# Kernel optimization log

Measured on AMD Instinct MI355X. Metric: run time of the kernel, lower is better.

## Reference

```python
import jax, jax.numpy as jnp
import numpy as np

VOCAB = 32000
HID = 1024
IN_DIM = 768
LAYERS = 2


def setup_inputs() -> dict:
    key = jax.random.key(0)
    ks = jax.random.split(key, 12)
    s = 0.02
    B, N, S = 8, 16, 512
    return {
        "concepts": jax.random.normal(ks[0], (B, N, IN_DIM), dtype=jnp.float32),
        "target_sequence": jax.random.randint(ks[1], (B, S), 0, VOCAB),
        "embedding": s * jax.random.normal(ks[2], (VOCAB, HID), dtype=jnp.float32),
        "w_ih": s * jax.random.normal(ks[3], (LAYERS, 3 * HID, HID), dtype=jnp.float32),
        "w_hh": s * jax.random.normal(ks[4], (LAYERS, 3 * HID, HID), dtype=jnp.float32),
        "b_ih": jnp.zeros((LAYERS, 3 * HID), dtype=jnp.float32),
        "b_hh": jnp.zeros((LAYERS, 3 * HID), dtype=jnp.float32),
        "fc_w": s * jax.random.normal(ks[5], (VOCAB, HID), dtype=jnp.float32),
        "fc_b": jnp.zeros((VOCAB,), dtype=jnp.float32),
        "c2h_w": s * jax.random.normal(ks[6], (HID * LAYERS, IN_DIM), dtype=jnp.float32),
        "c2h_b": jnp.zeros((HID * LAYERS,), dtype=jnp.float32),
    }


def _gru_layer(x, h0, w_ih, w_hh, b_ih, b_hh):
    # x: [B,S,H], h0: [B,H]. PyTorch GRU gate order: r, z, n.
    xg = jnp.einsum('bsh,gh->bsg', x, w_ih) + b_ih  # precompute input gates [B,S,3H]

    def step(h, xg_t):
        hg = h @ w_hh.T + b_hh
        xr, xz, xn = jnp.split(xg_t, 3, axis=-1)
        hr, hz, hn = jnp.split(hg, 3, axis=-1)
        r = jax.nn.sigmoid(xr + hr)
        z = jax.nn.sigmoid(xz + hz)
        n = jnp.tanh(xn + r * hn)
        h_new = (1.0 - z) * n + z * h
        return h_new, h_new

    _, ys = jax.lax.scan(step, h0, jnp.swapaxes(xg, 0, 1))  # [S,B,H]
    return jnp.swapaxes(ys, 0, 1)


def reference(concepts, target_sequence, embedding, w_ih, w_hh, b_ih, b_hh,
              fc_w, fc_b, c2h_w, c2h_b):
    B = concepts.shape[0]
    global_context = jnp.mean(concepts, axis=1)  # [B, D]
    h0 = (global_context @ c2h_w.T + c2h_b).reshape(B, LAYERS, HID)
    h0 = jnp.swapaxes(h0, 0, 1)  # [L, B, H] matching torch view(L, B, H)
    x = embedding[target_sequence]  # [B, S, H]
    for l in range(LAYERS):
        x = _gru_layer(x, h0[l], w_ih[l], w_hh[l], b_ih[l], b_hh[l])
    logits = jnp.einsum('bsh,vh->bsv', x, fc_w) + fc_b
    return logits
```

## Files before the change

kernel.cpp:

```cpp
#include <hip/hip_runtime.h>
#include <hip/hip_bf16.h>
#include <stdint.h>

#define B_ 8
#define S_ 512
#define H_ 1024
#define V_ 32000
#define D_ 768
#define G3H (3*H_)

typedef __bf16 bf16x8_t __attribute__((ext_vector_type(8)));
typedef float f32x4_t __attribute__((ext_vector_type(4)));

__device__ __forceinline__ unsigned short f2bf(float f) {
  unsigned int u = __float_as_uint(f);
  u += 0x7fffu + ((u >> 16) & 1u);
  return (unsigned short)(u >> 16);
}
__device__ __forceinline__ float fast_sigmoid(float x) {
  float e = __builtin_amdgcn_exp2f(x * -1.44269504088896340736f);
  return __builtin_amdgcn_rcpf(1.0f + e);
}
__device__ __forceinline__ float fast_tanh(float x) {
  float e = __builtin_amdgcn_exp2f(x * -2.88539008177792681472f);
  return 2.0f * __builtin_amdgcn_rcpf(1.0f + e) - 1.0f;
}

__global__ void zero_buf(uint4* __restrict__ p, int n) {
  int i = blockIdx.x * 256 + threadIdx.x;
  if (i < n) p[i] = uint4{0, 0, 0, 0};
}

__global__ void ctx_mean(const float* __restrict__ c, float* __restrict__ ctx) {
  int b = blockIdx.x;
  for (int d = threadIdx.x; d < D_; d += 256) {
    float s = 0.f;
    #pragma unroll
    for (int n = 0; n < 16; ++n) s += c[((size_t)b * 16 + n) * D_ + d];
    ctx[b * D_ + d] = s * (1.0f / 16.0f);
  }
}

__global__ void h0_compute(const float* __restrict__ ctx, const float* __restrict__ w,
                           const float* __restrict__ bias, float* __restrict__ h0l,
                           unsigned short* __restrict__ hb) {
  int o = blockIdx.x * 256 + threadIdx.x;
  int b = o >> 11, row = o & 2047;
  float s = bias[row];
  const float* cw = w + (size_t)row * D_;
  const float* cb = ctx + b * D_;
  for (int d = 0; d < D_; ++d) s += cb[d] * cw[d];
  int layer = row >> 10, u = row & 1023;
  h0l[((size_t)layer * 8 + b) * 1024 + u] = s;
  hb[(layer ? 24576 : 0) + b * 1024 + u] = f2bf(s);
}

__global__ void gather_embed(const int* __restrict__ seq, const float* __restrict__ emb,
                             unsigned short* __restrict__ x) {
  int r = blockIdx.x;
  int idx = seq[r];
  float4 v = ((const float4*)(emb + (size_t)idx * H_))[threadIdx.x];
  ushort4 o;
  o.x = f2bf(v.x); o.y = f2bf(v.y); o.z = f2bf(v.z); o.w = f2bf(v.w);
  ((ushort4*)(x + (size_t)r * H_))[threadIdx.x] = o;
}

__global__ void f32_to_bf16(const float* __restrict__ in, unsigned short* __restrict__ outp, long n4) {
  long i = blockIdx.x * (long)blockDim.x + threadIdx.x;
  long stride = (long)gridDim.x * blockDim.x;
  for (; i < n4; i += stride) {
    float4 v = ((const float4*)in)[i];
    ushort4 o;
    o.x = f2bf(v.x); o.y = f2bf(v.y); o.z = f2bf(v.z); o.w = f2bf(v.w);
    ((ushort4*)outp)[i] = o;
  }
}

__global__ __launch_bounds__(256) void gemm_bt_bf16(
    const unsigned short* __restrict__ A, const unsigned short* __restrict__ B,
    float* __restrict__ C, const float* __restrict__ bias,
    int M, int N, int K)
{
  __shared__ __align__(16) unsigned short As[128 * 32];
  __shared__ __align__(16) unsigned short Bs[128 * 32];
  const int tid = threadIdx.x;
  const int l = tid & 63;
  const int w = tid >> 6;
  const int wr = w >> 1, wc = w & 1;
  const long row0 = (long)blockIdx.y * 128;
  const long col0 = (long)blockIdx.x * 128;

  f32x4_t acc[4][4];
  #pragma unroll
  for (int m = 0; m < 4; ++m)
    #pragma unroll
    for (int n = 0; n < 4; ++n) acc[m][n] = (f32x4_t)0.0f;

  const int sr = tid >> 2;
  const int sc = (tid & 3) << 3;

  for (int kt = 0; kt < K; kt += 32) {
    __syncthreads();
    uint4 a0 = *(const uint4*)&A[(row0 + sr) * K + kt + sc];
    uint4 a1 = *(const uint4*)&A[(row0 + sr + 64) * K + kt + sc];
    uint4 b0 = *(const uint4*)&B[(col0 + sr) * K + kt + sc];
    uint4 b1 = *(const uint4*)&B[(col0 + sr + 64) * K + kt + sc];
    ((uint4*)As)[tid]       = a0;
    ((uint4*)As)[tid + 256] = a1;
    ((uint4*)Bs)[tid]       = b0;
    ((uint4*)Bs)[tid + 256] = b1;
    __syncthreads();

    bf16x8_t af[4], bfr[4];
    #pragma unroll
    for (int m = 0; m < 4; ++m)
      af[m] = *(const bf16x8_t*)&As[(wr * 64 + m * 16 + (l & 15)) * 32 + (l >> 4) * 8];
    #pragma unroll
    for (int n = 0; n < 4; ++n)
      bfr[n] = *(const bf16x8_t*)&Bs[(wc * 64 + n * 16 + (l & 15)) * 32 + (l >> 4) * 8];
    #pragma unroll
    for (int m = 0; m < 4; ++m)
      #pragma unroll
      for (int n = 0; n < 4; ++n)
        acc[m][n] = __builtin_amdgcn_mfma_f32_16x16x32_bf16(af[m], bfr[n], acc[m][n], 0, 0, 0);
  }

  #pragma unroll
  for (int n = 0; n < 4; ++n) {
    const long col = col0 + wc * 64 + n * 16 + (l & 15);
    const float bv = bias[col];
    #pragma unroll
    for (int m = 0; m < 4; ++m) {
      const long rbase = row0 + wr * 64 + m * 16 + ((l >> 4) << 2);
      #pragma unroll
      for (int v = 0; v < 4; ++v)
        C[(rbase + v) * (long)N + col] = acc[m][n][v] + bv;
    }
  }
}

__device__ __forceinline__ void load_wfrag3(const float* __restrict__ W, int j0, int w,
                                            int l15, int lhi, bf16x8_t wf[3][8]) {
  #pragma unroll
  for (int m = 0; m < 3; ++m) {
    const float* pr = W + (size_t)((m << 10) + j0 + l15) * 1024 + (w << 8) + (lhi << 3);
    #pragma unroll
    for (int c = 0; c < 8; ++c) {
      f32x4_t v0 = *(const f32x4_t*)(pr + (c << 5));
      f32x4_t v1 = *(const f32x4_t*)(pr + (c << 5) + 4);
      bf16x8_t f;
      f[0] = (__bf16)v0[0]; f[1] = (__bf16)v0[1]; f[2] = (__bf16)v0[2]; f[3] = (__bf16)v0[3];
      f[4] = (__bf16)v1[0]; f[5] = (__bf16)v1[1]; f[6] = (__bf16)v1[2]; f[7] = (__bf16)v1[3];
      wf[m][c] = f;
    }
  }
}

__global__ __launch_bounds__(256, 1) void gru_fused(
    const float* __restrict__ xg,
    const float* __restrict__ w_hh,
    const float* __restrict__ w_ih,
    const float* __restrict__ b_hh,
    const float* __restrict__ b_ih,
    const float* __restrict__ h0f,
    unsigned short* __restrict__ y,
    unsigned short* __restrict__ hb,
    int* __restrict__ fl)
{
  __shared__ __align__(16) float red[4 * 4 * 256];
  const int tid = threadIdx.x;
  const int blk = blockIdx.x;
  const int layer = blk >> 6;
  const int j0 = (blk & 63) << 4;
  const int w = tid >> 6;
  const int l = tid & 63;
  const int l15 = l & 15;
  const int lhi = l >> 4;
  const bool realrow = (l15 < 8);

  bf16x8_t wfh[3][8], wfi[3][8];
  #pragma unroll
  for (int m = 0; m < 3; ++m)
    #pragma unroll
    for (int c = 0; c < 8; ++c) wfi[m][c] = (bf16x8_t)(__bf16)0.0f;
  load_wfrag3(w_hh + (size_t)layer * G3H * H_, j0, w, l15, lhi, wfh);
  if (layer == 1) load_wfrag3(w_ih + (size_t)G3H * H_, j0, w, l15, lhi, wfi);

  const int up = tid & 7;
  const int b = tid >> 3;
  float gbr0 = 0.f, gbz0 = 0.f, gbnh0 = 0.f, gbni0 = 0.f, hp0 = 0.f;
  float gbr1 = 0.f, gbz1 = 0.f, gbnh1 = 0.f, gbni1 = 0.f, hp1 = 0.f;
  const float* xgp = nullptr;
  if (tid < 64) {
    const float* bhh_l = b_hh + (size_t)layer * G3H;
    const float* bih_l = b_ih + (size_t)layer * G3H;
    const int uj = j0 + 2 * up;
    float bhr0 = bhh_l[uj],     bhz0 = bhh_l[1024 + uj],     bhn0 = bhh_l[2048 + uj];
    float bhr1 = bhh_l[uj + 1], bhz1 = bhh_l[1024 + uj + 1], bhn1 = bhh_l[2048 + uj + 1];
    if (layer == 0) {
      gbr0 = bhr0; gbz0 = bhz0; gbnh0 = bhn0;
      gbr1 = bhr1; gbz1 = bhz1; gbnh1 = bhn1;
      xgp = xg + (size_t)(b * S_) * G3H + uj;
    } else {
      gbr0 = bhr0 + bih_l[uj];     gbz0 = bhz0 + bih_l[1024 + uj];
      gbnh0 = bhn0;                gbni0 = bih_l[2048 + uj];
      gbr1 = bhr1 + bih_l[uj + 1]; gbz1 = bhz1 + bih_l[1024 + uj + 1];
      gbnh1 = bhn1;                gbni1 = bih_l[2048 + uj + 1];
    }
    float2 h2 = *(const float2*)&h0f[(size_t)layer * 8192 + b * 1024 + uj];
    hp0 = h2.x; hp1 = h2.y;
  }

  unsigned short* const hb0 = hb;
  unsigned short* const hb1 = hb + 24576;
  const int frag = l15 * 1024 + (w << 8) + (lhi << 3);

  for (int e = 0; e <= S_; ++e) {
    const bool active = (layer == 0) ? (e < S_) : (e >= 1);
    const int t = (layer == 0) ? e : (e - 1);
    const int s3 = e % 3;

    if (tid >= 64 && tid < 192) {
      const int idx = tid - 64;
      const int thr = (idx < 64) ? e : ((layer == 0) ? (e - 1) : e);
      while (__hip_atomic_load(&fl[idx * 32], __ATOMIC_RELAXED, __HIP_MEMORY_SCOPE_AGENT) < thr)
        __builtin_amdgcn_s_sleep(1);
    }
    __syncthreads();

    f32x4_t accR = (f32x4_t)0.0f, accZ = (f32x4_t)0.0f;
    f32x4_t accNh = (f32x4_t)0.0f, accNi = (f32x4_t)0.0f;
    float2 xr2 = {0.f, 0.f}, xz2 = {0.f, 0.f}, xn2 = {0.f, 0.f};

    if (active) {
      f32x4_t hv[8], yv[8];
      #pragma unroll
      for (int c = 0; c < 8; ++c) { hv[c] = (f32x4_t)0.0f; yv[c] = (f32x4_t)0.0f; }
      if (realrow) {
        const unsigned short* hp = (layer == 0) ? (hb0 + s3 * 8192 + frag)
                                                : (hb1 + ((e + 1) & 1) * 8192 + frag);
        #pragma unroll
        for (int c = 0; c < 8; ++c)
          asm volatile("global_load_dwordx4 %0, %1, off offset:%2 sc0 sc1"
                       : "=v"(hv[c]) : "v"(hp), "i"(c * 64) : "memory");
        if (layer == 1) {
          const unsigned short* yp = hb0 + s3 * 8192 + frag;
          #pragma unroll
          for (int c = 0; c < 8; ++c)
            asm volatile("global_load_dwordx4 %0, %1, off offset:%2 sc0 sc1"
                         : "=v"(yv[c]) : "v"(yp), "i"(c * 64) : "memory");
        }
      }
      if (layer == 0 && tid < 64) {
        const float* p = xgp + (size_t)t * G3H;
        xr2 = *(const float2*)p;
        xz2 = *(const float2*)(p + 1024);
        xn2 = *(const float2*)(p + 2048);
      }
      asm volatile("s_waitcnt vmcnt(0)" ::: "memory");
      __builtin_amdgcn_sched_barrier(0);

      #pragma unroll
      for (int c = 0; c < 8; ++c) {
        bf16x8_t hf = __builtin_bit_cast(bf16x8_t, hv[c]);
        accR  = __builtin_amdgcn_mfma_f32_16x16x32_bf16(wfh[0][c], hf, accR,  0, 0, 0);
        accZ  = __builtin_amdgcn_mfma_f32_16x16x32_bf16(wfh[1][c], hf, accZ,  0, 0, 0);
        accNh = __builtin_amdgcn_mfma_f32_16x16x32_bf16(wfh[2][c], hf, accNh, 0, 0, 0);
      }
      if (layer == 1) {
        #pragma unroll
        for (int c = 0; c < 8; ++c) {
          bf16x8_t yf = __builtin_bit_cast(bf16x8_t, yv[c]);
          accR  = __builtin_amdgcn_mfma_f32_16x16x32_bf16(wfi[0][c], yf, accR,  0, 0, 0);
          accZ  = __builtin_amdgcn_mfma_f32_16x16x32_bf16(wfi[1][c], yf, accZ,  0, 0, 0);
          accNi = __builtin_amdgcn_mfma_f32_16x16x32_bf16(wfi[2][c], yf, accNi, 0, 0, 0);
        }
      }
      *(f32x4_t*)&red[(w * 4 + 0) * 256 + (l << 2)] = accR;
      *(f32x4_t*)&red[(w * 4 + 1) * 256 + (l << 2)] = accZ;
      *(f32x4_t*)&red[(w * 4 + 2) * 256 + (l << 2)] = accNh;
      *(f32x4_t*)&red[(w * 4 + 3) * 256 + (l << 2)] = accNi;
    }
    __syncthreads();

    if (active && tid < 64) {
      const int u0 = 2 * up, u1 = 2 * up + 1;
      const int i0 = ((((u0 >> 2) << 4) | b) << 2) + (u0 & 3);
      const int i1 = ((((u1 >> 2) << 4) | b) << 2) + (u1 & 3);
      float aR0 = 0.f, aZ0 = 0.f, aNh0 = 0.f, aNi0 = 0.f;
      float aR1 = 0.f, aZ1 = 0.f, aNh1 = 0.f, aNi1 = 0.f;
      #pragma unroll
      for (int ww = 0; ww < 4; ++ww) {
        const float* rw = red + ww * 1024;
        aR0  += rw[i0];        aR1  += rw[i1];
        aZ0  += rw[256 + i0];  aZ1  += rw[256 + i1];
        aNh0 += rw[512 + i0];  aNh1 += rw[512 + i1];
        aNi0 += rw[768 + i0];  aNi1 += rw[768 + i1];
      }
      float r0, z0, n0, r1, z1, n1;
      if (layer == 0) {
        r0 = fast_sigmoid(xr2.x + gbr0 + aR0);
        z0 = fast_sigmoid(xz2.x + gbz0 + aZ0);
        n0 = fast_tanh(xn2.x + r0 * (aNh0 + gbnh0));
        r1 = fast_sigmoid(xr2.y + gbr1 + aR1);
        z1 = fast_sigmoid(xz2.y + gbz1 + aZ1);
        n1 = fast_tanh(xn2.y + r1 * (aNh1 + gbnh1));
      } else {
        r0 = fast_sigmoid(aR0 + gbr0);
        z0 = fast_sigmoid(aZ0 + gbz0);
        n0 = fast_tanh(aNi0 + gbni0 + r0 * (aNh0 + gbnh0));
        r1 = fast_sigmoid(aR1 + gbr1);
        z1 = fast_sigmoid(aZ1 + gbz1);
        n1 = fast_tanh(aNi1 + gbni1 + r1 * (aNh1 + gbnh1));
      }
      hp0 = (1.0f - z0) * n0 + z0 * hp0;
      hp1 = (1.0f - z1) * n1 + z1 * hp1;
      uint32_t word = ((uint32_t)f2bf(hp1) << 16) | (uint32_t)f2bf(hp0);
      unsigned short* hdst = (layer == 0)
          ? (hb0 + ((e + 1) % 3) * 8192 + b * 1024 + j0 + 2 * up)
          : (hb1 + (e & 1) * 8192 + b * 1024 + j0 + 2 * up);
      if (layer == 1)
        *(uint32_t*)&y[(((size_t)(b * S_ + t)) << 10) + j0 + 2 * up] = word;
      asm volatile("global_store_dword %0, %1, off sc0 sc1"
                   :: "v"(hdst), "v"(word) : "memory");
    }
    asm volatile("s_waitcnt vmcnt(0)" ::: "memory");
    if (tid == 0)
      __hip_atomic_store(&fl[blk * 32], e + 1,
                         __ATOMIC_RELAXED, __HIP_MEMORY_SCOPE_AGENT);
  }
}

extern "C" void kernel_launch(void* const* d_in, const int* in_sizes, int n_in,
                              void* d_out, int out_size, void* d_ws, size_t ws_size,
                              hipStream_t stream) {
  (void)in_sizes; (void)n_in; (void)out_size; (void)ws_size;
  const float* concepts = (const float*)d_in[0];
  const int*   seq      = (const int*)d_in[1];
  const float* emb      = (const float*)d_in[2];
  const float* w_ih     = (const float*)d_in[3];
  const float* w_hh     = (const float*)d_in[4];
  const float* b_ih     = (const float*)d_in[5];
  const float* b_hh     = (const float*)d_in[6];
  const float* fc_w     = (const float*)d_in[7];
  const float* fc_b     = (const float*)d_in[8];
  const float* c2h_w    = (const float*)d_in[9];
  const float* c2h_b    = (const float*)d_in[10];
  float* out = (float*)d_out;

  char* ws = (char*)d_ws;
  size_t off = 0;
  auto alloc = [&](size_t bytes) {
    char* p = ws + off;
    off += (bytes + 255) & ~(size_t)255;
    return p;
  };
  unsigned short* xy   = (unsigned short*)alloc((size_t)B_ * S_ * H_ * 2);
  float*          xg   = (float*)alloc((size_t)B_ * S_ * G3H * 4);
  unsigned short* wihb = (unsigned short*)alloc((size_t)G3H * H_ * 2);
  unsigned short* fcwb = (unsigned short*)alloc((size_t)V_ * H_ * 2);
  float*          ctx  = (float*)alloc((size_t)B_ * D_ * 4);
  float*          h0l  = (float*)alloc((size_t)2 * B_ * H_ * 4);
  unsigned short* hb   = (unsigned short*)alloc((size_t)5 * 8 * 1024 * 2);
  int*            fl   = (int*)alloc((size_t)128 * 32 * 4);

  zero_buf<<<dim3(4), dim3(256), 0, stream>>>((uint4*)fl, 128 * 32 / 4);
  ctx_mean<<<dim3(8), dim3(256), 0, stream>>>(concepts, ctx);
  h0_compute<<<dim3(64), dim3(256), 0, stream>>>(ctx, c2h_w, c2h_b, h0l, hb);
  gather_embed<<<dim3(B_ * S_), dim3(256), 0, stream>>>(seq, emb, xy);
  f32_to_bf16<<<dim3(1024), dim3(256), 0, stream>>>(w_ih, wihb, (long)G3H * H_ / 4);
  f32_to_bf16<<<dim3(2048), dim3(256), 0, stream>>>(fc_w, fcwb, (long)V_ * H_ / 4);

  gemm_bt_bf16<<<dim3(G3H / 128, (B_ * S_) / 128), dim3(256), 0, stream>>>(
      xy, wihb, xg, b_ih, B_ * S_, G3H, H_);

  gru_fused<<<dim3(128), dim3(256), 0, stream>>>(
      xg, w_hh, w_ih, b_hh, b_ih, h0l, xy, hb, fl);

  gemm_bt_bf16<<<dim3(V_ / 128, (B_ * S_) / 128), dim3(256), 0, stream>>>(
      xy, fcwb, out, fc_b, B_ * S_, V_, H_);
}
```

Baseline: 2.505 ms.

## Tag hidden-state words with step ids to replace flag barriers in GRU recurrence

The persistent GRU kernel now splits work across 256 blocks of 8 hidden units each instead of 128 blocks of 16. It packs the gate rows into two MFMA tiles, so less of each tile is padding. Each published hidden-state value carries a 32-bit step tag, so consumers poll the data itself until all tags match. This replaces the per-block flag spin-waits and the store-drain before signalling. A flag is kept only to stop layer 0 from running too far ahead of layer 1, using a 4-deep ring. The trade-off is twice the bytes per hidden-state read, retry loops over the loads, and a correctness risk if the tag scheme or ring depth is wrong.

```diff
diff --git a/kernel.cpp b/kernel.cpp
--- a/kernel.cpp
+++ b/kernel.cpp
@@ -43,16 +43,21 @@
 
 __global__ void h0_compute(const float* __restrict__ ctx, const float* __restrict__ w,
                            const float* __restrict__ bias, float* __restrict__ h0l,
-                           unsigned short* __restrict__ hb) {
+                           uint32_t* __restrict__ hb0, uint32_t* __restrict__ hb1) {
   int o = blockIdx.x * 256 + threadIdx.x;
-  int b = o >> 11, row = o & 2047;
-  float s = bias[row];
-  const float* cw = w + (size_t)row * D_;
+  int layer = o >> 12, b = (o >> 9) & 7, p = o & 511;
+  int row = layer * 1024 + 2 * p;
+  float s0 = bias[row], s1 = bias[row + 1];
   const float* cb = ctx + b * D_;
-  for (int d = 0; d < D_; ++d) s += cb[d] * cw[d];
-  int layer = row >> 10, u = row & 1023;
-  h0l[((size_t)layer * 8 + b) * 1024 + u] = s;
-  hb[(layer ? 24576 : 0) + b * 1024 + u] = f2bf(s);
+  const float* w0 = w + (size_t)row * D_;
+  const float* w1 = w0 + D_;
+  for (int d = 0; d < D_; ++d) { s0 += cb[d] * w0[d]; s1 += cb[d] * w1[d]; }
+  h0l[layer * 8192 + b * 1024 + 2 * p] = s0;
+  h0l[layer * 8192 + b * 1024 + 2 * p + 1] = s1;
+  uint32_t vals = ((uint32_t)f2bf(s1) << 16) | (uint32_t)f2bf(s0);
+  uint32_t* dst = (layer ? hb1 : hb0) + ((size_t)b * 512 + p) * 2;
+  dst[0] = vals;
+  dst[1] = 0u;
 }
 
 __global__ void gather_embed(const int* __restrict__ seq, const float* __restrict__ emb,
@@ -139,21 +144,32 @@
   }
 }
 
-__device__ __forceinline__ void load_wfrag3(const float* __restrict__ W, int j0, int w,
-                                            int l15, int lhi, bf16x8_t wf[3][8]) {
+__device__ __forceinline__ void load_wfrag(const float* __restrict__ W, int j0, int w,
+                                           int l15, int lhi, bf16x8_t wf[2][8]) {
   #pragma unroll
-  for (int m = 0; m < 3; ++m) {
-    const float* pr = W + (size_t)((m << 10) + j0 + l15) * 1024 + (w << 8) + (lhi << 3);
+  for (int m = 0; m < 2; ++m) {
+    const int idx = m * 16 + l15;
+    const int gg = idx >> 3, uu = idx & 7;
     #pragma unroll
     for (int c = 0; c < 8; ++c) {
-      f32x4_t v0 = *(const f32x4_t*)(pr + (c << 5));
-      f32x4_t v1 = *(const f32x4_t*)(pr + (c << 5) + 4);
+      f32x4_t v0 = {0.f, 0.f, 0.f, 0.f}, v1 = {0.f, 0.f, 0.f, 0.f};
+      if (idx < 24) {
+        const float* p = W + (size_t)((gg << 10) + j0 + uu) * 1024
+                           + (w << 8) + (c << 5) + (lhi << 3);
+        v0 = *(const f32x4_t*)p;
+        v1 = *(const f32x4_t*)(p + 4);
+      }
       bf16x8_t f;
       f[0] = (__bf16)v0[0]; f[1] = (__bf16)v0[1]; f[2] = (__bf16)v0[2]; f[3] = (__bf16)v0[3];
       f[4] = (__bf16)v1[0]; f[5] = (__bf16)v1[1]; f[6] = (__bf16)v1[2]; f[7] = (__bf16)v1[3];
       wf[m][c] = f;
     }
   }
+}
+
+__device__ __forceinline__ bf16x8_t pack_frag(const uint4 a, const uint4 b) {
+  uint4 r; r.x = a.x; r.y = a.z; r.z = b.x; r.w = b.z;
+  return __builtin_bit_cast(bf16x8_t, r);
 }
 
 __global__ __launch_bounds__(256, 1) void gru_fused(
@@ -164,34 +180,35 @@
     const float* __restrict__ b_ih,
     const float* __restrict__ h0f,
     unsigned short* __restrict__ y,
-    unsigned short* __restrict__ hb,
+    uint32_t* __restrict__ hb0,
+    uint32_t* __restrict__ hb1,
     int* __restrict__ fl)
 {
-  __shared__ __align__(16) float red[4 * 4 * 256];
+  __shared__ __align__(16) float red[2 * 4 * 3 * 256];
   const int tid = threadIdx.x;
   const int blk = blockIdx.x;
-  const int layer = blk >> 6;
-  const int j0 = (blk & 63) << 4;
+  const int layer = blk >> 7;
+  const int j0 = (blk & 127) * 8;
   const int w = tid >> 6;
   const int l = tid & 63;
   const int l15 = l & 15;
   const int lhi = l >> 4;
   const bool realrow = (l15 < 8);
 
-  bf16x8_t wfh[3][8], wfi[3][8];
+  bf16x8_t wfh[2][8], wfi[2][8];
   #pragma unroll
-  for (int m = 0; m < 3; ++m)
+  for (int m = 0; m < 2; ++m)
     #pragma unroll
     for (int c = 0; c < 8; ++c) wfi[m][c] = (bf16x8_t)(__bf16)0.0f;
-  load_wfrag3(w_hh + (size_t)layer * G3H * H_, j0, w, l15, lhi, wfh);
-  if (layer == 1) load_wfrag3(w_ih + (size_t)G3H * H_, j0, w, l15, lhi, wfi);
-
-  const int up = tid & 7;
-  const int b = tid >> 3;
+  load_wfrag(w_hh + (size_t)layer * G3H * H_, j0, w, l15, lhi, wfh);
+  if (layer == 1) load_wfrag(w_ih + (size_t)G3H * H_, j0, w, l15, lhi, wfi);
+
+  const int up = tid & 3;
+  const int bb = tid >> 2;
   float gbr0 = 0.f, gbz0 = 0.f, gbnh0 = 0.f, gbni0 = 0.f, hp0 = 0.f;
   float gbr1 = 0.f, gbz1 = 0.f, gbnh1 = 0.f, gbni1 = 0.f, hp1 = 0.f;
   const float* xgp = nullptr;
-  if (tid < 64) {
+  if (tid < 32) {
     const float* bhh_l = b_hh + (size_t)layer * G3H;
     const float* bih_l = b_ih + (size_t)layer * G3H;
     const int uj = j0 + 2 * up;
@@ -200,102 +217,179 @@
     if (layer == 0) {
       gbr0 = bhr0; gbz0 = bhz0; gbnh0 = bhn0;
       gbr1 = bhr1; gbz1 = bhz1; gbnh1 = bhn1;
-      xgp = xg + (size_t)(b * S_) * G3H + uj;
+      xgp = xg + (size_t)(bb * S_) * G3H + uj;
     } else {
       gbr0 = bhr0 + bih_l[uj];     gbz0 = bhz0 + bih_l[1024 + uj];
       gbnh0 = bhn0;                gbni0 = bih_l[2048 + uj];
       gbr1 = bhr1 + bih_l[uj + 1]; gbz1 = bhz1 + bih_l[1024 + uj + 1];
       gbnh1 = bhn1;                gbni1 = bih_l[2048 + uj + 1];
     }
-    float2 h2 = *(const float2*)&h0f[(size_t)layer * 8192 + b * 1024 + uj];
+    float2 h2 = *(const float2*)&h0f[(size_t)layer * 8192 + bb * 1024 + uj];
     hp0 = h2.x; hp1 = h2.y;
   }
 
-  unsigned short* const hb0 = hb;
-  unsigned short* const hb1 = hb + 24576;
-  const int frag = l15 * 1024 + (w << 8) + (lhi << 3);
+  const int lane_off = ((l15 << 9) + (w << 7) + (lhi << 2)) * 2;
+  const bool fduty = (layer == 0) && (tid >= 64 && tid < 192);
+  int* flp = fl + (tid - 64) * 32;
+
+  __syncthreads();
 
   for (int e = 0; e <= S_; ++e) {
-    const bool active = (layer == 0) ? (e < S_) : (e >= 1);
+    const bool act = (layer == 0) ? (e < S_) : (e >= 1);
     const int t = (layer == 0) ? e : (e - 1);
-    const int s3 = e % 3;
-
-    if (tid >= 64 && tid < 192) {
-      const int idx = tid - 64;
-      const int thr = (idx < 64) ? e : ((layer == 0) ? (e - 1) : e);
-      while (__hip_atomic_load(&fl[idx * 32], __ATOMIC_RELAXED, __HIP_MEMORY_SCOPE_AGENT) < thr)
-        __builtin_amdgcn_s_sleep(1);
+    const int p = e & 1;
+
+    f32x4_t a0h = (f32x4_t)0.0f, a1h = (f32x4_t)0.0f, a1i = (f32x4_t)0.0f;
+    float2 xr2 = {0.f, 0.f}, xz2 = {0.f, 0.f}, xn2 = {0.f, 0.f};
+    int flv = 0x7fffffff;
+
+    if (act) {
+      if (layer == 0) {
+        if (fduty)
+          asm volatile("global_load_dword %0, %1, off sc0 sc1"
+                       : "=v"(flv) : "v"(flp) : "memory");
+        if (tid < 32) {
+          const float* xp = xgp + (size_t)t * G3H;
+          xr2 = *(const float2*)xp;
+          xz2 = *(const float2*)(xp + 1024);
+          xn2 = *(const float2*)(xp + 2048);
+        }
+        const uint32_t* rb = hb0 + (size_t)(e & 3) * 8192 + lane_off;
+        const uint32_t tg = (uint32_t)e;
+        uint4 q0[8], q1[8];
+        #pragma unroll
+        for (int c = 0; c < 8; ++c) { q0[c] = uint4{0,0,0,0}; q1[c] = uint4{0,0,0,0}; }
+        if (realrow) {
+          #pragma unroll
+          for (int c = 0; c < 8; ++c)
+            asm volatile("global_load_dwordx4 %0, %2, off offset:%3 sc0 sc1\n\t"
+                         "global_load_dwordx4 %1, %2, off offset:%4 sc0 sc1"
+                         : "=&v"(q0[c]), "=&v"(q1[c])
+                         : "v"(rb), "i"(c * 128), "i"(c * 128 + 16) : "memory");
+        }
+        asm volatile("s_waitcnt vmcnt(0)" ::: "memory");
+        __builtin_amdgcn_sched_barrier(0);
+        for (;;) {
+          uint32_t bad = 0;
+          if (realrow) {
+            #pragma unroll
+            for (int c = 0; c < 8; ++c)
+              bad |= (q0[c].y ^ tg) | (q0[c].w ^ tg) | (q1[c].y ^ tg) | (q1[c].w ^ tg);
+          }
+          if (!__any(bad != 0)) break;
+          if (realrow) {
+            #pragma unroll
+            for (int c = 0; c < 8; ++c)
+              asm volatile("global_load_dwordx4 %0, %2, off offset:%3 sc0 sc1\n\t"
+                           "global_load_dwordx4 %1, %2, off offset:%4 sc0 sc1"
+                           : "=&v"(q0[c]), "=&v"(q1[c])
+                           : "v"(rb), "i"(c * 128), "i"(c * 128 + 16) : "memory");
+          }
+          asm volatile("s_waitcnt vmcnt(0)" ::: "memory");
+          __builtin_amdgcn_sched_barrier(0);
+        }
+        if (fduty) {
+          while (flv < e - 3) {
+            __builtin_amdgcn_s_sleep(1);
+            flv = __hip_atomic_load(flp, __ATOMIC_RELAXED, __HIP_MEMORY_SCOPE_AGENT);
+          }
+        }
+        __builtin_amdgcn_sched_barrier(0);
+        #pragma unroll
+        for (int c = 0; c < 8; ++c) {
+          bf16x8_t hf = pack_frag(q0[c], q1[c]);
+          a0h = __builtin_amdgcn_mfma_f32_16x16x32_bf16(wfh[0][c], hf, a0h, 0, 0, 0);
+          a1h = __builtin_amdgcn_mfma_f32_16x16x32_bf16(wfh[1][c], hf, a1h, 0, 0, 0);
+        }
+      } else {
+        const uint32_t* yb = hb0 + (size_t)(e & 3) * 8192 + lane_off;
+        const uint32_t* hbm = hb1 + (size_t)((e + 1) & 1) * 8192 + lane_off;
+        const uint32_t tgy = (uint32_t)e, tgh = (uint32_t)(e - 1);
+        uint4 qy0[8], qy1[8], qh0[8], qh1[8];
+        #pragma unroll
+        for (int c = 0; c < 8; ++c) {
+          qy0[c] = uint4{0,0,0,0}; qy1[c] = uint4{0,0,0,0};
+          qh0[c] = uint4{0,0,0,0}; qh1[c] = uint4{0,0,0,0};
+        }
+        if (realrow) {
+          #pragma unroll
+          for (int c = 0; c < 8; ++c)
+            asm volatile("global_load_dwordx4 %0, %2, off offset:%3 sc0 sc1\n\t"
+                         "global_load_dwordx4 %1, %2, off offset:%4 sc0 sc1"
+                         : "=&v"(qy0[c]), "=&v"(qy1[c])
+                         : "v"(yb), "i"(c * 128), "i"(c * 128 + 16) : "memory");
+          #pragma unroll
+          for (int c = 0; c < 8; ++c)
+            asm volatile("global_load_dwordx4 %0, %2, off offset:%3 sc0 sc1\n\t"
+                         "global_load_dwordx4 %1, %2, off offset:%4 sc0 sc1"
+                         : "=&v"(qh0[c]), "=&v"(qh1[c])
+                         : "v"(hbm), "i"(c * 128), "i"(c * 128 + 16) : "memory");
+        }
+        asm volatile("s_waitcnt vmcnt(0)" ::: "memory");
+        __builtin_amdgcn_sched_barrier(0);
+        for (;;) {
+          uint32_t bad = 0;
+          if (realrow) {
+            #pragma unroll
+            for (int c = 0; c < 8; ++c) {
+              bad |= (qy0[c].y ^ tgy) | (qy0[c].w ^ tgy) | (qy1[c].y ^ tgy) | (qy1[c].w ^ tgy);
+              bad |= (qh0[c].y ^ tgh) | (qh0[c].w ^ tgh) | (qh1[c].y ^ tgh) | (qh1[c].w ^ tgh);
+            }
+          }
+          if (!__any(bad != 0)) break;
+          if (realrow) {
+            #pragma unroll
+            for (int c = 0; c < 8; ++c)
+              asm volatile("global_load_dwordx4 %0, %2, off offset:%3 sc0 sc1\n\t"
+                           "global_load_dwordx4 %1, %2, off offset:%4 sc0 sc1"
+                           : "=&v"(qy0[c]), "=&v"(qy1[c])
+                           : "v"(yb), "i"(c * 128), "i"(c * 128 + 16) : "memory");
+            #pragma unroll
+            for (int c = 0; c < 8; ++c)
+              asm volatile("global_load_dwordx4 %0, %2, off offset:%3 sc0 sc1\n\t"
+                           "global_load_dwordx4 %1, %2, off offset:%4 sc0 sc1"
+                           : "=&v"(qh0[c]), "=&v"(qh1[c])
+                           : "v"(hbm), "i"(c * 128), "i"(c * 128 + 16) : "memory");
+          }
+          asm volatile("s_waitcnt vmcnt(0)" ::: "memory");
+          __builtin_amdgcn_sched_barrier(0);
+        }
+        __builtin_amdgcn_sched_barrier(0);
+        #pragma unroll
+        for (int c = 0; c < 8; ++c) {
+          bf16x8_t hf = pack_frag(qh0[c], qh1[c]);
+          bf16x8_t yf = pack_frag(qy0[c], qy1[c]);
+          a0h = __builtin_amdgcn_mfma_f32_16x16x32_bf16(wfh[0][c], hf, a0h, 0, 0, 0);
+          a1h = __builtin_amdgcn_mfma_f32_16x16x32_bf16(wfh[1][c], hf, a1h, 0, 0, 0);
+          a0h = __builtin_amdgcn_mfma_f32_16x16x32_bf16(wfi[0][c], yf, a0h, 0, 0, 0);
+          a1i = __builtin_amdgcn_mfma_f32_16x16x32_bf16(wfi[1][c], yf, a1i, 0, 0, 0);
+        }
+      }
+      float* rp = red + p * 3072 + (w * 3) * 256 + (l << 2);
+      *(f32x4_t*)(rp)       = a0h;
+      *(f32x4_t*)(rp + 256) = a1h;
+      *(f32x4_t*)(rp + 512) = a1i;
     }
     __syncthreads();
 
-    f32x4_t accR = (f32x4_t)0.0f, accZ = (f32x4_t)0.0f;
-    f32x4_t accNh = (f32x4_t)0.0f, accNi = (f32x4_t)0.0f;
-    float2 xr2 = {0.f, 0.f}, xz2 = {0.f, 0.f}, xn2 = {0.f, 0.f};
-
-    if (active) {
-      f32x4_t hv[8], yv[8];
-      #pragma unroll
-      for (int c = 0; c < 8; ++c) { hv[c] = (f32x4_t)0.0f; yv[c] = (f32x4_t)0.0f; }
-      if (realrow) {
-        const unsigned short* hp = (layer == 0) ? (hb0 + s3 * 8192 + frag)
-                                                : (hb1 + ((e + 1) & 1) * 8192 + frag);
-        #pragma unroll
-        for (int c = 0; c < 8; ++c)
-          asm volatile("global_load_dwordx4 %0, %1, off offset:%2 sc0 sc1"
-                       : "=v"(hv[c]) : "v"(hp), "i"(c * 64) : "memory");
-        if (layer == 1) {
-          const unsigned short* yp = hb0 + s3 * 8192 + frag;
-          #pragma unroll
-          for (int c = 0; c < 8; ++c)
-            asm volatile("global_load_dwordx4 %0, %1, off offset:%2 sc0 sc1"
-                         : "=v"(yv[c]) : "v"(yp), "i"(c * 64) : "memory");
-        }
-      }
-      if (layer == 0 && tid < 64) {
-        const float* p = xgp + (size_t)t * G3H;
-        xr2 = *(const float2*)p;
-        xz2 = *(const float2*)(p + 1024);
-        xn2 = *(const float2*)(p + 2048);
-      }
-      asm volatile("s_waitcnt vmcnt(0)" ::: "memory");
-      __builtin_amdgcn_sched_barrier(0);
-
-      #pragma unroll
-      for (int c = 0; c < 8; ++c) {
-        bf16x8_t hf = __builtin_bit_cast(bf16x8_t, hv[c]);
-        accR  = __builtin_amdgcn_mfma_f32_16x16x32_bf16(wfh[0][c], hf, accR,  0, 0, 0);
-        accZ  = __builtin_amdgcn_mfma_f32_16x16x32_bf16(wfh[1][c], hf, accZ,  0, 0, 0);
-        accNh = __builtin_amdgcn_mfma_f32_16x16x32_bf16(wfh[2][c], hf, accNh, 0, 0, 0);
-      }
-      if (layer == 1) {
-        #pragma unroll
-        for (int c = 0; c < 8; ++c) {
-          bf16x8_t yf = __builtin_bit_cast(bf16x8_t, yv[c]);
-          accR  = __builtin_amdgcn_mfma_f32_16x16x32_bf16(wfi[0][c], yf, accR,  0, 0, 0);
-          accZ  = __builtin_amdgcn_mfma_f32_16x16x32_bf16(wfi[1][c], yf, accZ,  0, 0, 0);
-          accNi = __builtin_amdgcn_mfma_f32_16x16x32_bf16(wfi[2][c], yf, accNi, 0, 0, 0);
-        }
-      }
-      *(f32x4_t*)&red[(w * 4 + 0) * 256 + (l << 2)] = accR;
-      *(f32x4_t*)&red[(w * 4 + 1) * 256 + (l << 2)] = accZ;
-      *(f32x4_t*)&red[(w * 4 + 2) * 256 + (l << 2)] = accNh;
-      *(f32x4_t*)&red[(w * 4 + 3) * 256 + (l << 2)] = accNi;
-    }
-    __syncthreads();
-
-    if (active && tid < 64) {
-      const int u0 = 2 * up, u1 = 2 * up + 1;
-      const int i0 = ((((u0 >> 2) << 4) | b) << 2) + (u0 & 3);
-      const int i1 = ((((u1 >> 2) << 4) | b) << 2) + (u1 & 3);
+    if (layer == 1 && act && tid == 0)
+      __hip_atomic_store(&fl[(blk & 127) * 32], e,
+                         __ATOMIC_RELAXED, __HIP_MEMORY_SCOPE_AGENT);
+
+    if (act && tid < 32) {
+      const int u0 = 2 * up, u1 = u0 + 1;
+      const int i0 = ((((u0 >> 2) << 4) | bb) << 2) + (u0 & 3);
+      const int i1 = ((((u1 >> 2) << 4) | bb) << 2) + (u1 & 3);
+      const float* rbase = red + p * 3072;
       float aR0 = 0.f, aZ0 = 0.f, aNh0 = 0.f, aNi0 = 0.f;
       float aR1 = 0.f, aZ1 = 0.f, aNh1 = 0.f, aNi1 = 0.f;
       #pragma unroll
       for (int ww = 0; ww < 4; ++ww) {
-        const float* rw = red + ww * 1024;
+        const float* rw = rbase + ww * 768;
         aR0  += rw[i0];        aR1  += rw[i1];
-        aZ0  += rw[256 + i0];  aZ1  += rw[256 + i1];
-        aNh0 += rw[512 + i0];  aNh1 += rw[512 + i1];
-        aNi0 += rw[768 + i0];  aNi1 += rw[768 + i1];
+        aZ0  += rw[128 + i0];  aZ1  += rw[128 + i1];
+        aNh0 += rw[256 + i0];  aNh1 += rw[256 + i1];
+        aNi0 += rw[512 + i0];  aNi1 += rw[512 + i1];
       }
       float r0, z0, n0, r1, z1, n1;
       if (layer == 0) {
@@ -315,19 +409,17 @@
       }
       hp0 = (1.0f - z0) * n0 + z0 * hp0;
       hp1 = (1.0f - z1) * n1 + z1 * hp1;
-      uint32_t word = ((uint32_t)f2bf(hp1) << 16) | (uint32_t)f2bf(hp0);
-      unsigned short* hdst = (layer == 0)
-          ? (hb0 + ((e + 1) % 3) * 8192 + b * 1024 + j0 + 2 * up)
-          : (hb1 + (e & 1) * 8192 + b * 1024 + j0 + 2 * up);
+      uint32_t vals = ((uint32_t)f2bf(hp1) << 16) | (uint32_t)f2bf(hp0);
+      const uint32_t wtag = (layer == 0) ? (uint32_t)(e + 1) : (uint32_t)e;
+      unsigned long long chunk = ((unsigned long long)wtag << 32) | vals;
+      uint32_t* hdst = (layer == 0)
+          ? (hb0 + (size_t)((e + 1) & 3) * 8192 + ((size_t)bb * 512 + (j0 >> 1) + up) * 2)
+          : (hb1 + (size_t)(e & 1) * 8192 + ((size_t)bb * 512 + (j0 >> 1) + up) * 2);
       if (layer == 1)
-        *(uint32_t*)&y[(((size_t)(b * S_ + t)) << 10) + j0 + 2 * up] = word;
-      asm volatile("global_store_dword %0, %1, off sc0 sc1"
-                   :: "v"(hdst), "v"(word) : "memory");
+        *(uint32_t*)&y[(((size_t)(bb * S_ + t)) << 10) + j0 + 2 * up] = vals;
+      asm volatile("global_store_dwordx2 %0, %1, off sc0 sc1"
+                   :: "v"(hdst), "v"(chunk) : "memory");
     }
-    asm volatile("s_waitcnt vmcnt(0)" ::: "memory");
-    if (tid == 0)
-      __hip_atomic_store(&fl[blk * 32], e + 1,
-                         __ATOMIC_RELAXED, __HIP_MEMORY_SCOPE_AGENT);
   }
 }
 
@@ -361,12 +453,13 @@
   unsigned short* fcwb = (unsigned short*)alloc((size_t)V_ * H_ * 2);
   float*          ctx  = (float*)alloc((size_t)B_ * D_ * 4);
   float*          h0l  = (float*)alloc((size_t)2 * B_ * H_ * 4);
-  unsigned short* hb   = (unsigned short*)alloc((size_t)5 * 8 * 1024 * 2);
+  uint32_t*       hb0  = (uint32_t*)alloc((size_t)4 * 8192 * 4);
+  uint32_t*       hb1  = (uint32_t*)alloc((size_t)2 * 8192 * 4);
   int*            fl   = (int*)alloc((size_t)128 * 32 * 4);
 
   zero_buf<<<dim3(4), dim3(256), 0, stream>>>((uint4*)fl, 128 * 32 / 4);
   ctx_mean<<<dim3(8), dim3(256), 0, stream>>>(concepts, ctx);
-  h0_compute<<<dim3(64), dim3(256), 0, stream>>>(ctx, c2h_w, c2h_b, h0l, hb);
+  h0_compute<<<dim3(32), dim3(256), 0, stream>>>(ctx, c2h_w, c2h_b, h0l, hb0, hb1);
   gather_embed<<<dim3(B_ * S_), dim3(256), 0, stream>>>(seq, emb, xy);
   f32_to_bf16<<<dim3(1024), dim3(256), 0, stream>>>(w_ih, wihb, (long)G3H * H_ / 4);
   f32_to_bf16<<<dim3(2048), dim3(256), 0, stream>>>(fc_w, fcwb, (long)V_ * H_ / 4);
@@ -374,8 +467,8 @@
   gemm_bt_bf16<<<dim3(G3H / 128, (B_ * S_) / 128), dim3(256), 0, stream>>>(
       xy, wihb, xg, b_ih, B_ * S_, G3H, H_);
 
-  gru_fused<<<dim3(128), dim3(256), 0, stream>>>(
-      xg, w_hh, w_ih, b_hh, b_ih, h0l, xy, hb, fl);
+  gru_fused<<<dim3(256), dim3(256), 0, stream>>>(
+      xg, w_hh, w_ih, b_hh, b_ih, h0l, xy, hb0, hb1, fl);
 
   gemm_bt_bf16<<<dim3(V_ / 128, (B_ * S_) / 128), dim3(256), 0, stream>>>(
       xy, fcwb, out, fc_b, B_ * S_, V_, H_);
```

Measured after the change: 4.897 ms. 1.95x slower.
